# Kernel tuning notes

Measured on AMD Instinct MI355X. Metric: run time of the kernel, lower is better.

## Reference

```python
import jax, jax.numpy as jnp
import numpy as np

B, S, D = 8, 1024, 768
H, DH = 8, 96          # number_of_heads, head_outdim = D // H
DFF = 4 * D            # mlp hidden
EPS = 1e-5


def _p(key, shape, scale=0.02):
    return (jax.random.normal(key, shape, dtype=jnp.float32) * scale)


def setup_inputs() -> dict:
    key = jax.random.key(0)
    ks = jax.random.split(key, 16)
    return {
        "h": jax.random.normal(ks[0], (B, S, D), dtype=jnp.float32),
        "x": jax.random.normal(ks[1], (B, S, D), dtype=jnp.float32),
        # SLN 1: scalar gamma/beta + LayerNorm affine
        "g1": jnp.ones((), jnp.float32), "be1": jnp.zeros((), jnp.float32),
        "ln1_w": jnp.ones((D,), jnp.float32), "ln1_b": jnp.zeros((D,), jnp.float32),
        # SLN 2
        "g2": jnp.ones((), jnp.float32), "be2": jnp.zeros((), jnp.float32),
        "ln2_w": jnp.ones((D,), jnp.float32), "ln2_b": jnp.zeros((D,), jnp.float32),
        # MSA projections (stored as [in, out] for x @ W)
        "Wq": _p(ks[2], (D, H * DH)), "bq": jnp.zeros((H * DH,), jnp.float32),
        "Wk": _p(ks[3], (D, H * DH)), "bk": jnp.zeros((H * DH,), jnp.float32),
        "Wv": _p(ks[4], (D, H * DH)), "bv": jnp.zeros((H * DH,), jnp.float32),
        "Wo": _p(ks[5], (H * DH, D)), "bo": jnp.zeros((D,), jnp.float32),
        # MLP: D -> 4D -> D, relu
        "W1": _p(ks[6], (D, DFF)), "b1": jnp.zeros((DFF,), jnp.float32),
        "W2": _p(ks[7], (DFF, D)), "b2": jnp.zeros((D,), jnp.float32),
    }


def _sln(h, x, gamma, beta, w, b):
    # SLN(h, x) = gamma * x * LayerNorm(h) + beta * x
    mu = jnp.mean(h, axis=-1, keepdims=True)
    var = jnp.var(h, axis=-1, keepdims=True)
    ln = (h - mu) * jax.lax.rsqrt(var + EPS) * w + b
    return gamma * x * ln + beta * x


def _l2_msa(h, Wq, bq, Wk, bk, Wv, bv, Wo, bo):
    # L2-distance multi-head self-attention (lp=2)
    def heads(W, bias):
        y = h @ W + bias                      # [B,S,H*DH]
        return y.reshape(B, S, H, DH).transpose(0, 2, 1, 3)  # [B,H,S,DH]
    q, k, v = heads(Wq, bq), heads(Wk, bk), heads(Wv, bv)
    # pairwise L2 distances via the quadratic expansion (avoids [B,H,S,S,DH])
    q2 = jnp.sum(q * q, axis=-1)              # [B,H,S]
    k2 = jnp.sum(k * k, axis=-1)              # [B,H,S]
    qk = jnp.einsum("bhsd,bhtd->bhst", q, k)  # [B,H,S,S]
    d2 = jnp.maximum(q2[..., :, None] + k2[..., None, :] - 2.0 * qk, 0.0)
    dist = jnp.sqrt(d2)                       # cdist(q, k, p=2)
    attn = jax.nn.softmax(-dist / np.sqrt(DH), axis=-1)
    out = jnp.einsum("bhst,bhtd->bhsd", attn, v)  # [B,H,S,DH]
    out = out.transpose(0, 2, 1, 3).reshape(B, S, H * DH)
    return out @ Wo + bo


def reference(h, x, g1, be1, ln1_w, ln1_b, g2, be2, ln2_w, ln2_b,
              Wq, bq, Wk, bk, Wv, bv, Wo, bo, W1, b1, W2, b2):
    h1 = _sln(h, x, g1, be1, ln1_w, ln1_b)
    htmp = _l2_msa(h1, Wq, bq, Wk, bk, Wv, bv, Wo, bo) + h   # dropout_rate=0 -> identity
    h2 = _sln(htmp, x, g2, be2, ln2_w, ln2_b)
    hf = jax.nn.relu(h2 @ W1 + b1) @ W2 + b2 + htmp
    return (x, hf)
```

## Files before the change

### kernel.cpp

```cpp
#include <hip/hip_runtime.h>
#include <math.h>

#define B_ 8
#define S_ 1024
#define D_ 768
#define H_ 8
#define DH_ 96
#define DFF_ 3072
#define NTOK (B_*S_)
#define QKVW 2304
#define EPS_ 1e-5f

typedef __attribute__((ext_vector_type(4))) float f4;
typedef __attribute__((ext_vector_type(4))) int i4;
typedef __attribute__((ext_vector_type(8))) __bf16 bf16x8;
typedef __attribute__((ext_vector_type(4))) unsigned short us4;
typedef __attribute__((ext_vector_type(8))) unsigned short us8;

static __device__ __forceinline__ unsigned short f2bf(float f) {
    unsigned int u = __builtin_bit_cast(unsigned int, f);
    u += 0x7fffu + ((u >> 16) & 1u);
    return (unsigned short)(u >> 16);
}
static __device__ __forceinline__ float bf2f(unsigned short u) {
    unsigned int x = ((unsigned int)u) << 16;
    return __builtin_bit_cast(float, x);
}

#define GLOBAL_LOAD_LDS16(g, l) \
    __builtin_amdgcn_global_load_lds((const __attribute__((address_space(1))) unsigned int*)(g), \
                                     (__attribute__((address_space(3))) unsigned int*)(l), 16, 0, 0)

__global__ __launch_bounds__(192) void sln_kernel(
    const float* __restrict__ h, const float* __restrict__ x,
    const float* __restrict__ gamma, const float* __restrict__ beta,
    const float* __restrict__ w, const float* __restrict__ bvec,
    unsigned short* __restrict__ out_bf, float* __restrict__ xcopy)
{
    int row = blockIdx.x;
    int t = threadIdx.x;
    const float4* h4 = (const float4*)(h + (size_t)row * D_);
    const float4* x4 = (const float4*)(x + (size_t)row * D_);
    float4 hv = h4[t];
    float s  = hv.x + hv.y + hv.z + hv.w;
    float ss = hv.x*hv.x + hv.y*hv.y + hv.z*hv.z + hv.w*hv.w;
    #pragma unroll
    for (int off = 32; off > 0; off >>= 1) {
        s  += __shfl_down(s, off);
        ss += __shfl_down(ss, off);
    }
    __shared__ float red[2][3];
    int wid = t >> 6;
    if ((t & 63) == 0) { red[0][wid] = s; red[1][wid] = ss; }
    __syncthreads();
    float sum   = red[0][0] + red[0][1] + red[0][2];
    float sumsq = red[1][0] + red[1][1] + red[1][2];
    float mu  = sum * (1.0f / D_);
    float var = sumsq * (1.0f / D_) - mu * mu;
    float rstd = rsqrtf(var + EPS_);
    float g = gamma[0], be = beta[0];
    float4 wv = ((const float4*)w)[t];
    float4 bv = ((const float4*)bvec)[t];
    float4 xv = x4[t];
    us4 o;
    o.x = f2bf(xv.x * (g * ((hv.x - mu) * rstd * wv.x + bv.x) + be));
    o.y = f2bf(xv.y * (g * ((hv.y - mu) * rstd * wv.y + bv.y) + be));
    o.z = f2bf(xv.z * (g * ((hv.z - mu) * rstd * wv.z + bv.z) + be));
    o.w = f2bf(xv.w * (g * ((hv.w - mu) * rstd * wv.w + bv.w) + be));
    *(us4*)(out_bf + (size_t)row * D_ + t * 4) = o;
    if (xcopy) ((float4*)(xcopy + (size_t)row * D_))[t] = xv;
}

__global__ __launch_bounds__(256) void prep_all_kernel(
    const float* __restrict__ Wq, const float* __restrict__ Wk,
    const float* __restrict__ Wv, const float* __restrict__ Wo,
    const float* __restrict__ W1, const float* __restrict__ W2,
    const float* __restrict__ bq, const float* __restrict__ bk, const float* __restrict__ bv,
    unsigned short* __restrict__ Wqkvt, unsigned short* __restrict__ Wot,
    unsigned short* __restrict__ W1t, unsigned short* __restrict__ W2t,
    float* __restrict__ bqkv)
{
    int id = blockIdx.x;
    int tx = threadIdx.x, ty = threadIdx.y;
    if (id >= 6912) {
        int i = (id - 6912) * 256 + ty * 32 + tx;
        if (i < QKVW) {
            float v = (i < 768) ? bq[i] : (i < 1536) ? -2.f * bk[i - 768] : bv[i - 1536];
            bqkv[i] = v;
        }
        return;
    }
    const float* in; unsigned short* out; int K, N, nbx, rel;
    float scl = 1.f;
    if (id < 1728)      { int m = id / 576; rel = id % 576;
                          in = (m == 0) ? Wq : (m == 1) ? Wk : Wv;
                          if (m == 1) scl = -2.f;
                          out = Wqkvt + (size_t)m * 768 * 768; K = 768; N = 768; nbx = 24; }
    else if (id < 2304) { rel = id - 1728; in = Wo; out = Wot;  K = 768;  N = 768;  nbx = 24; }
    else if (id < 4608) { rel = id - 2304; in = W1; out = W1t;  K = 768;  N = 3072; nbx = 96; }
    else                { rel = id - 4608; in = W2; out = W2t;  K = 3072; N = 768;  nbx = 24; }
    int n0 = (rel % nbx) * 32, k0 = (rel / nbx) * 32;
    __shared__ float tile[32][33];
    #pragma unroll
    for (int r = 0; r < 4; r++)
        tile[ty + r * 8][tx] = in[(size_t)(k0 + ty + r * 8) * N + n0 + tx];
    __syncthreads();
    #pragma unroll
    for (int r = 0; r < 4; r++)
        out[(size_t)(n0 + ty + r * 8) * K + k0 + tx] = f2bf(scl * tile[tx][ty + r * 8]);
}

template<int OUT_BF16, int RELU>
__global__ __launch_bounds__(256) void gemm_mfma_kernel(
    const unsigned short* __restrict__ A, const unsigned short* __restrict__ Bt,
    const float* __restrict__ bias, const float* __restrict__ resid,
    void* __restrict__ Cout, int M, int N, int K)
{
    __shared__ unsigned short Asm[2][128 * 32];
    __shared__ unsigned short Bsm[2][128 * 32];

    int t = threadIdx.x;
    int lane = t & 63, wv = t >> 6;
    int wm = wv & 1, wn = wv >> 1;
    int l16 = lane & 15, quad = lane >> 4;

    int bm = blockIdx.x * 128;
    int bn = blockIdx.y * 128;

    const unsigned short* Abase = A  + (size_t)bm * K;
    const unsigned short* Bbase = Bt + (size_t)bn * K;

    int fl0 = t, fl1 = 256 + t;
    int r0 = fl0 >> 2, lg0 = (fl0 ^ (fl0 >> 3)) & 3;
    int r1 = fl1 >> 2, lg1 = (fl1 ^ (fl1 >> 3)) & 3;

    f4 acc[4][4] = {};

    GLOBAL_LOAD_LDS16(Abase + (size_t)r0 * K + lg0 * 8, &Asm[0][fl0 * 8]);
    GLOBAL_LOAD_LDS16(Abase + (size_t)r1 * K + lg1 * 8, &Asm[0][fl1 * 8]);
    GLOBAL_LOAD_LDS16(Bbase + (size_t)r0 * K + lg0 * 8, &Bsm[0][fl0 * 8]);
    GLOBAL_LOAD_LDS16(Bbase + (size_t)r1 * K + lg1 * 8, &Bsm[0][fl1 * 8]);
    __syncthreads();

    int nk = K >> 5;
    int cur = 0;
    for (int it = 0; it < nk; ++it) {
        if (it + 1 < nk) {
            int k0 = (it + 1) << 5;
            GLOBAL_LOAD_LDS16(Abase + (size_t)r0 * K + k0 + lg0 * 8, &Asm[cur ^ 1][fl0 * 8]);
            GLOBAL_LOAD_LDS16(Abase + (size_t)r1 * K + k0 + lg1 * 8, &Asm[cur ^ 1][fl1 * 8]);
            GLOBAL_LOAD_LDS16(Bbase + (size_t)r0 * K + k0 + lg0 * 8, &Bsm[cur ^ 1][fl0 * 8]);
            GLOBAL_LOAD_LDS16(Bbase + (size_t)r1 * K + k0 + lg1 * 8, &Bsm[cur ^ 1][fl1 * 8]);
        }

        bf16x8 xf[4], wf[4];
        #pragma unroll
        for (int i = 0; i < 4; i++) {
            int m = wm * 64 + i * 16 + l16;
            int p = (quad ^ (m >> 1)) & 3;
            xf[i] = __builtin_bit_cast(bf16x8, *(const i4*)&Asm[cur][m * 32 + p * 8]);
        }
        #pragma unroll
        for (int j = 0; j < 4; j++) {
            int n = wn * 64 + j * 16 + l16;
            int p = (quad ^ (n >> 1)) & 3;
            wf[j] = __builtin_bit_cast(bf16x8, *(const i4*)&Bsm[cur][n * 32 + p * 8]);
        }
        #pragma unroll
        for (int j = 0; j < 4; j++)
            #pragma unroll
            for (int i = 0; i < 4; i++)
                acc[j][i] = __builtin_amdgcn_mfma_f32_16x16x32_bf16(wf[j], xf[i], acc[j][i], 0, 0, 0);

        __syncthreads();
        cur ^= 1;
    }

    #pragma unroll
    for (int i = 0; i < 4; i++) {
        int rowg = bm + wm * 64 + i * 16 + l16;
        #pragma unroll
        for (int j = 0; j < 4; j++) {
            int colg0 = bn + wn * 64 + j * 16 + quad * 4;
            f4 v = acc[j][i];
            f4 b4 = *(const f4*)&bias[colg0];
            v += b4;
            if (RELU) {
                #pragma unroll
                for (int r = 0; r < 4; r++) v[r] = fmaxf(v[r], 0.f);
            }
            if (resid) {
                f4 r4 = *(const f4*)&resid[(size_t)rowg * N + colg0];
                v += r4;
            }
            if (OUT_BF16) {
                us4 o;
                o.x = f2bf(v[0]); o.y = f2bf(v[1]); o.z = f2bf(v[2]); o.w = f2bf(v[3]);
                *(us4*)((unsigned short*)Cout + (size_t)rowg * N + colg0) = o;
            } else {
                *(f4*)((float*)Cout + (size_t)rowg * N + colg0) = v;
            }
        }
    }
}

template<int OUT_BF16, int RELU>
__global__ __launch_bounds__(256) void gemm_mfma_n64_kernel(
    const unsigned short* __restrict__ A, const unsigned short* __restrict__ Bt,
    const float* __restrict__ bias, const float* __restrict__ resid,
    void* __restrict__ Cout, int M, int N, int K)
{
    __shared__ unsigned short Asm[2][128 * 64];
    __shared__ unsigned short Bsm[2][64 * 64];

    int t = threadIdx.x;
    int lane = t & 63, wv = t >> 6;
    int wm = wv & 1, wn = wv >> 1;
    int l16 = lane & 15, quad = lane >> 4;

    int bm = blockIdx.x * 128;
    int bn = blockIdx.y * 64;

    const unsigned short* Abase = A  + (size_t)bm * K;
    const unsigned short* Bbase = Bt + (size_t)bn * K;

    int ar[4], alg[4], br[2], blg[2];
    #pragma unroll
    for (int i = 0; i < 4; i++) {
        int fl = t + i * 256;
        ar[i] = fl >> 3; alg[i] = (fl ^ (fl >> 3)) & 7;
    }
    #pragma unroll
    for (int i = 0; i < 2; i++) {
        int fl = t + i * 256;
        br[i] = fl >> 3; blg[i] = (fl ^ (fl >> 3)) & 7;
    }

    f4 acc[2][4] = {};

    #pragma unroll
    for (int i = 0; i < 4; i++)
        GLOBAL_LOAD_LDS16(Abase + (size_t)ar[i] * K + alg[i] * 8, &Asm[0][(t + i * 256) * 8]);
    #pragma unroll
    for (int i = 0; i < 2; i++)
        GLOBAL_LOAD_LDS16(Bbase + (size_t)br[i] * K + blg[i] * 8, &Bsm[0][(t + i * 256) * 8]);
    __syncthreads();

    int nk = K >> 6;
    int cur = 0;
    for (int it = 0; it < nk; ++it) {
        if (it + 1 < nk) {
            int k0 = (it + 1) << 6;
            #pragma unroll
            for (int i = 0; i < 4; i++)
                GLOBAL_LOAD_LDS16(Abase + (size_t)ar[i] * K + k0 + alg[i] * 8, &Asm[cur ^ 1][(t + i * 256) * 8]);
            #pragma unroll
            for (int i = 0; i < 2; i++)
                GLOBAL_LOAD_LDS16(Bbase + (size_t)br[i] * K + k0 + blg[i] * 8, &Bsm[cur ^ 1][(t + i * 256) * 8]);
        }

        #pragma unroll
        for (int kk = 0; kk < 2; kk++) {
            bf16x8 xf[4], wf[2];
            #pragma unroll
            for (int i = 0; i < 4; i++) {
                int m = wm * 64 + i * 16 + l16;
                int p = ((kk * 4 + quad) ^ (m & 7)) & 7;
                xf[i] = __builtin_bit_cast(bf16x8, *(const i4*)&Asm[cur][m * 64 + p * 8]);
            }
            #pragma unroll
            for (int j = 0; j < 2; j++) {
                int n = wn * 32 + j * 16 + l16;
                int p = ((kk * 4 + quad) ^ (n & 7)) & 7;
                wf[j] = __builtin_bit_cast(bf16x8, *(const i4*)&Bsm[cur][n * 64 + p * 8]);
            }
            #pragma unroll
            for (int j = 0; j < 2; j++)
                #pragma unroll
                for (int i = 0; i < 4; i++)
                    acc[j][i] = __builtin_amdgcn_mfma_f32_16x16x32_bf16(wf[j], xf[i], acc[j][i], 0, 0, 0);
        }

        __syncthreads();
        cur ^= 1;
    }

    #pragma unroll
    for (int i = 0; i < 4; i++) {
        int rowg = bm + wm * 64 + i * 16 + l16;
        #pragma unroll
        for (int j = 0; j < 2; j++) {
            int colg0 = bn + wn * 32 + j * 16 + quad * 4;
            f4 v = acc[j][i];
            f4 b4 = *(const f4*)&bias[colg0];
            v += b4;
            if (RELU) {
                #pragma unroll
                for (int r = 0; r < 4; r++) v[r] = fmaxf(v[r], 0.f);
            }
            if (resid) {
                f4 r4 = *(const f4*)&resid[(size_t)rowg * N + colg0];
                v += r4;
            }
            if (OUT_BF16) {
                us4 o;
                o.x = f2bf(v[0]); o.y = f2bf(v[1]); o.z = f2bf(v[2]); o.w = f2bf(v[3]);
                *(us4*)((unsigned short*)Cout + (size_t)rowg * N + colg0) = o;
            } else {
                *(f4*)((float*)Cout + (size_t)rowg * N + colg0) = v;
            }
        }
    }
}

__global__ __launch_bounds__(256) void norms_kernel(
    const unsigned short* __restrict__ qkv, float* __restrict__ q2g, float* __restrict__ k2g)
{
    int row = blockIdx.x;
    int t = threadIdx.x;
    int hh = t >> 5, l32 = t & 31;
    const unsigned short* base = qkv + (size_t)row * QKVW + hh * DH_ + l32 * 3;
    float qs = 0.f, ks = 0.f;
    #pragma unroll
    for (int e = 0; e < 3; e++) {
        float qv = bf2f(base[e]);
        float kv = bf2f(base[768 + e]);
        qs += qv * qv; ks += kv * kv;
    }
    #pragma unroll
    for (int off = 16; off > 0; off >>= 1) {
        qs += __shfl_xor(qs, off, 32);
        ks += __shfl_xor(ks, off, 32);
    }
    if (l32 == 0) {
        int b = row >> 10, s = row & 1023;
        int idx = (b * H_ + hh) * S_ + s;
        q2g[idx] = qs; k2g[idx] = ks * 0.25f;
    }
}

__global__ __launch_bounds__(256) void vtrans_kernel(
    const unsigned short* __restrict__ qkv, unsigned short* __restrict__ vt)
{
    __shared__ unsigned short Vl[64][100];
    int blk = blockIdx.x;
    int bh = blk >> 4, kt = blk & 15;
    int b = bh >> 3, hh = bh & 7;
    int t = threadIdx.x;
    int key = t >> 2, qc = t & 3;
    const unsigned short* src = qkv + ((size_t)(b * S_ + kt * 64 + key)) * QKVW + 1536 + hh * DH_;
    #pragma unroll
    for (int i = 0; i < 3; i++) {
        int chunk = qc + i * 4;
        us8 v = *(const us8*)(src + chunk * 8);
        #pragma unroll
        for (int e = 0; e < 8; e++) Vl[key][chunk * 8 + e] = v[e];
    }
    __syncthreads();
    unsigned short* dst = vt + (size_t)blk * 7168;
    #pragma unroll
    for (int r = 0; r < 3; r++) {
        int c = r * 256 + t;
        int vd = c >> 3, kc = c & 7;
        us8 o;
        #pragma unroll
        for (int j = 0; j < 8; j++) o[j] = Vl[kc * 8 + j][vd];
        *(us8*)(dst + vd * 72 + kc * 8) = o;
    }
}

__global__ __launch_bounds__(256, 4) void attn_mfma_kernel(
    const unsigned short* __restrict__ qkv,
    const unsigned short* __restrict__ vt,
    const float* __restrict__ q2g, const float* __restrict__ k2g,
    unsigned short* __restrict__ outb)
{
    __shared__ unsigned short Klds[64 * 96];
    __shared__ unsigned short Vlds[7168];
    __shared__ unsigned short Plds[4][16 * 72];

    int t = threadIdx.x;
    int lane = t & 63, w = t >> 6;
    int l16 = lane & 15, quad = lane >> 4;

    int bid = blockIdx.x;
    int slot = bid >> 3;
    int bh = (bid & 7) * 8 + (slot >> 4);
    int qt = slot & 15;
    int b = bh >> 3, hh = bh & 7;

    int qrow0 = qt * 64 + w * 16;

    const unsigned short* qb = qkv + ((size_t)(b * S_ + qrow0)) * QKVW + hh * DH_;
    bf16x8 qf[3];
    #pragma unroll
    for (int d = 0; d < 3; d++)
        qf[d] = __builtin_bit_cast(bf16x8,
            *(const i4*)(qb + (size_t)l16 * QKVW + d * 32 + quad * 8));

    float q2n = q2g[bh * S_ + qrow0 + l16];

    float lsum = 0.f;
    f4 Oacc[6] = {};

    const float cexp = 0.14724445f;

    const unsigned short* kgb = qkv + ((size_t)(b * S_)) * QKVW + 768 + hh * DH_;
    const unsigned short* vgb0 = vt + (size_t)(bh * 16) * 7168;
    const float* k2base = k2g + bh * S_;

    for (int it = 0; it < 16; it++) {
        float4 k2f[4];
        #pragma unroll
        for (int kt2 = 0; kt2 < 4; kt2++)
            k2f[kt2] = *(const float4*)(k2base + it * 64 + kt2 * 16 + quad * 4);

        __syncthreads();
        #pragma unroll
        for (int r = 0; r < 3; r++) {
            int c = r * 256 + t;
            int key = c & 63, dc = c >> 6;
            GLOBAL_LOAD_LDS16(kgb + ((size_t)(it * 64 + key)) * QKVW + dc * 8, &Klds[c * 8]);
        }
        const unsigned short* vgb = vgb0 + (size_t)it * 7168;
        #pragma unroll
        for (int r = 0; r < 3; r++)
            GLOBAL_LOAD_LDS16(vgb + (r * 256 + t) * 8, &Vlds[(r * 256 + t) * 8]);
        if (t < 128)
            GLOBAL_LOAD_LDS16(vgb + (768 + t) * 8, &Vlds[(768 + t) * 8]);
        __syncthreads();

        const unsigned short* kB = &Klds[quad * 512 + l16 * 8];
        #pragma unroll
        for (int kt2 = 0; kt2 < 4; kt2++) {
            const unsigned short* kp = kB + kt2 * 128;
            bf16x8 kf0 = __builtin_bit_cast(bf16x8, *(const i4*)(kp));
            bf16x8 kf1 = __builtin_bit_cast(bf16x8, *(const i4*)(kp + 2048));
            bf16x8 kf2 = __builtin_bit_cast(bf16x8, *(const i4*)(kp + 4096));
            f4 a = {k2f[kt2].x + q2n, k2f[kt2].y + q2n, k2f[kt2].z + q2n, k2f[kt2].w + q2n};
            a = __builtin_amdgcn_mfma_f32_16x16x32_bf16(kf0, qf[0], a, 0, 0, 0);
            a = __builtin_amdgcn_mfma_f32_16x16x32_bf16(kf1, qf[1], a, 0, 0, 0);
            a = __builtin_amdgcn_mfma_f32_16x16x32_bf16(kf2, qf[2], a, 0, 0, 0);
            #pragma unroll
            for (int r2 = 0; r2 < 4; r2++) {
                float d2 = fmaxf(a[r2], 0.f);
                float p = exp2f(-__builtin_amdgcn_sqrtf(d2) * cexp);
                lsum += p;
                a[r2] = p;
            }
            unsigned int plo, phi;
            asm("v_cvt_pk_bf16_f32 %0, %1, %2" : "=v"(plo) : "v"(a[0]), "v"(a[1]));
            asm("v_cvt_pk_bf16_f32 %0, %1, %2" : "=v"(phi) : "v"(a[2]), "v"(a[3]));
            uint2 pkd; pkd.x = plo; pkd.y = phi;
            *(uint2*)&Plds[w][l16 * 72 + kt2 * 16 + quad * 4] = pkd;
        }
        bf16x8 pa0 = __builtin_bit_cast(bf16x8, *(const i4*)&Plds[w][l16 * 72 + quad * 8]);
        bf16x8 pa1 = __builtin_bit_cast(bf16x8, *(const i4*)&Plds[w][l16 * 72 + 32 + quad * 8]);
        #pragma unroll
        for (int vtl = 0; vtl < 6; vtl++) {
            bf16x8 vf0 = __builtin_bit_cast(bf16x8, *(const i4*)&Vlds[(vtl * 16 + l16) * 72 + quad * 8]);
            bf16x8 vf1 = __builtin_bit_cast(bf16x8, *(const i4*)&Vlds[(vtl * 16 + l16) * 72 + 32 + quad * 8]);
            Oacc[vtl] = __builtin_amdgcn_mfma_f32_16x16x32_bf16(pa0, vf0, Oacc[vtl], 0, 0, 0);
            Oacc[vtl] = __builtin_amdgcn_mfma_f32_16x16x32_bf16(pa1, vf1, Oacc[vtl], 0, 0, 0);
        }
    }
    lsum += __shfl_xor(lsum, 16, 64);
    lsum += __shfl_xor(lsum, 32, 64);
    float inv_l = 1.f / lsum;
    f4 iv;
    #pragma unroll
    for (int r2 = 0; r2 < 4; r2++)
        iv[r2] = __shfl(inv_l, quad * 4 + r2, 64);
    #pragma unroll
    for (int vtl = 0; vtl < 6; vtl++)
        #pragma unroll
        for (int r2 = 0; r2 < 4; r2++) {
            int row = b * S_ + qrow0 + quad * 4 + r2;
            outb[(size_t)row * D_ + hh * DH_ + vtl * 16 + l16] = f2bf(Oacc[vtl][r2] * iv[r2]);
        }
}

extern "C" void kernel_launch(void* const* d_in, const int* in_sizes, int n_in,
                              void* d_out, int out_size, void* d_ws, size_t ws_size,
                              hipStream_t stream)
{
    const float* h    = (const float*)d_in[0];
    const float* x    = (const float*)d_in[1];
    const float* g1   = (const float*)d_in[2];
    const float* be1  = (const float*)d_in[3];
    const float* ln1w = (const float*)d_in[4];
    const float* ln1b = (const float*)d_in[5];
    const float* g2   = (const float*)d_in[6];
    const float* be2  = (const float*)d_in[7];
    const float* ln2w = (const float*)d_in[8];
    const float* ln2b = (const float*)d_in[9];
    const float* Wq   = (const float*)d_in[10];
    const float* bq   = (const float*)d_in[11];
    const float* Wk   = (const float*)d_in[12];
    const float* bk   = (const float*)d_in[13];
    const float* Wv   = (const float*)d_in[14];
    const float* bv   = (const float*)d_in[15];
    const float* Wo   = (const float*)d_in[16];
    const float* bo   = (const float*)d_in[17];
    const float* W1   = (const float*)d_in[18];
    const float* b1   = (const float*)d_in[19];
    const float* W2   = (const float*)d_in[20];
    const float* b2   = (const float*)d_in[21];

    float* out = (float*)d_out;
    char* wsb = (char*)d_ws;
    const size_t ND = (size_t)NTOK * D_;

    size_t off = 0;
    unsigned short* W1t = (unsigned short*)(wsb + off); off += 4718592;
    unsigned short* W2t = (unsigned short*)(wsb + off); off += 4718592;
    float* bqkv = (float*)(wsb + off);                  off += 16384;
    float* htmp = (float*)(wsb + off);                  off += ND * 4;
    float* q2g  = (float*)(wsb + off);                  off += (size_t)B_ * H_ * S_ * 4;
    float* k2g  = (float*)(wsb + off);                  off += (size_t)B_ * H_ * S_ * 4;
    unsigned short* h2b = (unsigned short*)(wsb + off); off += ND * 2;
    size_t pool0 = off;
    unsigned short* Wqkvt = (unsigned short*)(wsb + off); off += 3538944;
    unsigned short* Wot   = (unsigned short*)(wsb + off); off += 1179648;
    unsigned short* h1b   = (unsigned short*)(wsb + off); off += ND * 2;
    unsigned short* vtg   = (unsigned short*)(wsb + off); off += (size_t)1024 * 14336;
    unsigned short* qkvb  = (unsigned short*)(wsb + off); off += (size_t)NTOK * QKVW * 2;
    unsigned short* attnb   = h1b;
    unsigned short* hiddenb = (unsigned short*)(wsb + pool0);

    prep_all_kernel<<<6921, dim3(32, 8), 0, stream>>>(
        Wq, Wk, Wv, Wo, W1, W2, bq, bk, bv, Wqkvt, Wot, W1t, W2t, bqkv);

    sln_kernel<<<NTOK, 192, 0, stream>>>(h, x, g1, be1, ln1w, ln1b, h1b, out);

    gemm_mfma_kernel<1, 0><<<dim3(NTOK/128, QKVW/128), 256, 0, stream>>>(
        h1b, Wqkvt, bqkv, nullptr, qkvb, NTOK, QKVW, D_);

    norms_kernel<<<NTOK, 256, 0, stream>>>(qkvb, q2g, k2g);
    vtrans_kernel<<<1024, 256, 0, stream>>>(qkvb, vtg);

    attn_mfma_kernel<<<1024, 256, 0, stream>>>(qkvb, vtg, q2g, k2g, attnb);

    gemm_mfma_n64_kernel<0, 0><<<dim3(NTOK/128, D_/64), 256, 0, stream>>>(
        attnb, Wot, bo, h, htmp, NTOK, D_, D_);

    sln_kernel<<<NTOK, 192, 0, stream>>>(htmp, x, g2, be2, ln2w, ln2b, h2b, nullptr);

    gemm_mfma_kernel<1, 1><<<dim3(NTOK/128, DFF_/128), 256, 0, stream>>>(
        h2b, W1t, b1, nullptr, hiddenb, NTOK, DFF_, D_);
    gemm_mfma_n64_kernel<0, 0><<<dim3(NTOK/128, D_/64), 256, 0, stream>>>(
        hiddenb, W2t, b2, htmp, out + ND, NTOK, D_, DFF_);

    (void)in_sizes; (void)n_in; (void)out_size; (void)ws_size;
}
```

Before: 429.3 us.

## Double-buffer K/V tiles and process two query fragments per wave in attention

The L2 attention kernel now has each wave handle 32 query rows (two 16-row fragments), so each K/V tile loaded into LDS is reused across twice as many queries and the grid is halved to 512 blocks. K and V tiles are double-buffered, with the next tile's global-to-LDS load issued before computing on the current one, which removes one barrier per iteration and overlaps loads with compute. The cost is more registers (launch bounds relaxed to 2 blocks per SM), more LDS per block, and fewer blocks in flight.

```diff
diff --git a/kernel.cpp b/kernel.cpp
--- a/kernel.cpp
+++ b/kernel.cpp
@@ -369,15 +369,15 @@
     }
 }
 
-__global__ __launch_bounds__(256, 4) void attn_mfma_kernel(
+__global__ __launch_bounds__(256, 2) void attn_mfma_kernel(
     const unsigned short* __restrict__ qkv,
     const unsigned short* __restrict__ vt,
     const float* __restrict__ q2g, const float* __restrict__ k2g,
     unsigned short* __restrict__ outb)
 {
-    __shared__ unsigned short Klds[64 * 96];
-    __shared__ unsigned short Vlds[7168];
-    __shared__ unsigned short Plds[4][16 * 72];
+    __shared__ unsigned short Klds[2][6144];
+    __shared__ unsigned short Vlds[2][7168];
+    __shared__ unsigned short Plds[4][2][16 * 72];
 
     int t = threadIdx.x;
     int lane = t & 63, w = t >> 6;
@@ -385,23 +385,28 @@
 
     int bid = blockIdx.x;
     int slot = bid >> 3;
-    int bh = (bid & 7) * 8 + (slot >> 4);
-    int qt = slot & 15;
+    int bh = (bid & 7) * 8 + (slot >> 3);
+    int qt = slot & 7;
     int b = bh >> 3, hh = bh & 7;
 
-    int qrow0 = qt * 64 + w * 16;
-
-    const unsigned short* qb = qkv + ((size_t)(b * S_ + qrow0)) * QKVW + hh * DH_;
-    bf16x8 qf[3];
-    #pragma unroll
-    for (int d = 0; d < 3; d++)
-        qf[d] = __builtin_bit_cast(bf16x8,
-            *(const i4*)(qb + (size_t)l16 * QKVW + d * 32 + quad * 8));
-
-    float q2n = q2g[bh * S_ + qrow0 + l16];
-
-    float lsum = 0.f;
-    f4 Oacc[6] = {};
+    int qrowW = qt * 128 + w * 32;
+
+    const unsigned short* qb = qkv + ((size_t)(b * S_ + qrowW)) * QKVW + hh * DH_;
+    bf16x8 qf[2][3];
+    #pragma unroll
+    for (int f = 0; f < 2; f++)
+        #pragma unroll
+        for (int d = 0; d < 3; d++)
+            qf[f][d] = __builtin_bit_cast(bf16x8,
+                *(const i4*)(qb + (size_t)(f * 16 + l16) * QKVW + d * 32 + quad * 8));
+
+    float q2n[2];
+    #pragma unroll
+    for (int f = 0; f < 2; f++)
+        q2n[f] = q2g[bh * S_ + qrowW + f * 16 + l16];
+
+    float lsum0 = 0.f, lsum1 = 0.f;
+    f4 Oacc[2][6] = {};
 
     const float cexp = 0.14724445f;
 
@@ -409,75 +414,101 @@
     const unsigned short* vgb0 = vt + (size_t)(bh * 16) * 7168;
     const float* k2base = k2g + bh * S_;
 
+    int kkey = t & 63;
+    #define ATTN_STAGE(bb, itv)                                                   \
+        {                                                                         \
+            _Pragma("unroll")                                                     \
+            for (int r = 0; r < 3; r++) {                                         \
+                int c = r * 256 + t;                                              \
+                int dc = c >> 6;                                                  \
+                GLOBAL_LOAD_LDS16(kgb + ((size_t)((itv) * 64 + kkey)) * QKVW + dc * 8, \
+                                  &Klds[bb][c * 8]);                              \
+            }                                                                     \
+            const unsigned short* vgb = vgb0 + (size_t)(itv) * 7168;              \
+            _Pragma("unroll")                                                     \
+            for (int r = 0; r < 3; r++)                                           \
+                GLOBAL_LOAD_LDS16(vgb + (r * 256 + t) * 8, &Vlds[bb][(r * 256 + t) * 8]); \
+            if (t < 128)                                                          \
+                GLOBAL_LOAD_LDS16(vgb + (768 + t) * 8, &Vlds[bb][(768 + t) * 8]); \
+        }
+
+    ATTN_STAGE(0, 0);
+    __syncthreads();
+
     for (int it = 0; it < 16; it++) {
+        int cur = it & 1;
+        if (it) __syncthreads();
+        if (it + 1 < 16) ATTN_STAGE(cur ^ 1, it + 1);
+
         float4 k2f[4];
         #pragma unroll
         for (int kt2 = 0; kt2 < 4; kt2++)
             k2f[kt2] = *(const float4*)(k2base + it * 64 + kt2 * 16 + quad * 4);
 
-        __syncthreads();
-        #pragma unroll
-        for (int r = 0; r < 3; r++) {
-            int c = r * 256 + t;
-            int key = c & 63, dc = c >> 6;
-            GLOBAL_LOAD_LDS16(kgb + ((size_t)(it * 64 + key)) * QKVW + dc * 8, &Klds[c * 8]);
-        }
-        const unsigned short* vgb = vgb0 + (size_t)it * 7168;
-        #pragma unroll
-        for (int r = 0; r < 3; r++)
-            GLOBAL_LOAD_LDS16(vgb + (r * 256 + t) * 8, &Vlds[(r * 256 + t) * 8]);
-        if (t < 128)
-            GLOBAL_LOAD_LDS16(vgb + (768 + t) * 8, &Vlds[(768 + t) * 8]);
-        __syncthreads();
-
-        const unsigned short* kB = &Klds[quad * 512 + l16 * 8];
+        const unsigned short* kB = &Klds[cur][quad * 512 + l16 * 8];
         #pragma unroll
         for (int kt2 = 0; kt2 < 4; kt2++) {
             const unsigned short* kp = kB + kt2 * 128;
             bf16x8 kf0 = __builtin_bit_cast(bf16x8, *(const i4*)(kp));
             bf16x8 kf1 = __builtin_bit_cast(bf16x8, *(const i4*)(kp + 2048));
             bf16x8 kf2 = __builtin_bit_cast(bf16x8, *(const i4*)(kp + 4096));
-            f4 a = {k2f[kt2].x + q2n, k2f[kt2].y + q2n, k2f[kt2].z + q2n, k2f[kt2].w + q2n};
-            a = __builtin_amdgcn_mfma_f32_16x16x32_bf16(kf0, qf[0], a, 0, 0, 0);
-            a = __builtin_amdgcn_mfma_f32_16x16x32_bf16(kf1, qf[1], a, 0, 0, 0);
-            a = __builtin_amdgcn_mfma_f32_16x16x32_bf16(kf2, qf[2], a, 0, 0, 0);
+            #pragma unroll
+            for (int f = 0; f < 2; f++) {
+                f4 a = {k2f[kt2].x + q2n[f], k2f[kt2].y + q2n[f],
+                        k2f[kt2].z + q2n[f], k2f[kt2].w + q2n[f]};
+                a = __builtin_amdgcn_mfma_f32_16x16x32_bf16(kf0, qf[f][0], a, 0, 0, 0);
+                a = __builtin_amdgcn_mfma_f32_16x16x32_bf16(kf1, qf[f][1], a, 0, 0, 0);
+                a = __builtin_amdgcn_mfma_f32_16x16x32_bf16(kf2, qf[f][2], a, 0, 0, 0);
+                #pragma unroll
+                for (int r2 = 0; r2 < 4; r2++) {
+                    float d2 = fmaxf(a[r2], 0.f);
+                    float p = exp2f(-__builtin_amdgcn_sqrtf(d2) * cexp);
+                    if (f == 0) lsum0 += p; else lsum1 += p;
+                    a[r2] = p;
+                }
+                unsigned int plo, phi;
+                asm("v_cvt_pk_bf16_f32 %0, %1, %2" : "=v"(plo) : "v"(a[0]), "v"(a[1]));
+                asm("v_cvt_pk_bf16_f32 %0, %1, %2" : "=v"(phi) : "v"(a[2]), "v"(a[3]));
+                uint2 pkd; pkd.x = plo; pkd.y = phi;
+                *(uint2*)&Plds[w][f][l16 * 72 + kt2 * 16 + quad * 4] = pkd;
+            }
+        }
+        bf16x8 pa[2][2];
+        #pragma unroll
+        for (int f = 0; f < 2; f++) {
+            pa[f][0] = __builtin_bit_cast(bf16x8, *(const i4*)&Plds[w][f][l16 * 72 + quad * 8]);
+            pa[f][1] = __builtin_bit_cast(bf16x8, *(const i4*)&Plds[w][f][l16 * 72 + 32 + quad * 8]);
+        }
+        #pragma unroll
+        for (int vtl = 0; vtl < 6; vtl++) {
+            bf16x8 vf0 = __builtin_bit_cast(bf16x8, *(const i4*)&Vlds[cur][(vtl * 16 + l16) * 72 + quad * 8]);
+            bf16x8 vf1 = __builtin_bit_cast(bf16x8, *(const i4*)&Vlds[cur][(vtl * 16 + l16) * 72 + 32 + quad * 8]);
+            #pragma unroll
+            for (int f = 0; f < 2; f++) {
+                Oacc[f][vtl] = __builtin_amdgcn_mfma_f32_16x16x32_bf16(pa[f][0], vf0, Oacc[f][vtl], 0, 0, 0);
+                Oacc[f][vtl] = __builtin_amdgcn_mfma_f32_16x16x32_bf16(pa[f][1], vf1, Oacc[f][vtl], 0, 0, 0);
+            }
+        }
+    }
+    #pragma unroll
+    for (int f = 0; f < 2; f++) {
+        float ls = (f == 0) ? lsum0 : lsum1;
+        ls += __shfl_xor(ls, 16, 64);
+        ls += __shfl_xor(ls, 32, 64);
+        float inv_l = 1.f / ls;
+        f4 iv;
+        #pragma unroll
+        for (int r2 = 0; r2 < 4; r2++)
+            iv[r2] = __shfl(inv_l, quad * 4 + r2, 64);
+        #pragma unroll
+        for (int vtl = 0; vtl < 6; vtl++)
             #pragma unroll
             for (int r2 = 0; r2 < 4; r2++) {
-                float d2 = fmaxf(a[r2], 0.f);
-                float p = exp2f(-__builtin_amdgcn_sqrtf(d2) * cexp);
-                lsum += p;
-                a[r2] = p;
-            }
-            unsigned int plo, phi;
-            asm("v_cvt_pk_bf16_f32 %0, %1, %2" : "=v"(plo) : "v"(a[0]), "v"(a[1]));
-            asm("v_cvt_pk_bf16_f32 %0, %1, %2" : "=v"(phi) : "v"(a[2]), "v"(a[3]));
-            uint2 pkd; pkd.x = plo; pkd.y = phi;
-            *(uint2*)&Plds[w][l16 * 72 + kt2 * 16 + quad * 4] = pkd;
-        }
-        bf16x8 pa0 = __builtin_bit_cast(bf16x8, *(const i4*)&Plds[w][l16 * 72 + quad * 8]);
-        bf16x8 pa1 = __builtin_bit_cast(bf16x8, *(const i4*)&Plds[w][l16 * 72 + 32 + quad * 8]);
-        #pragma unroll
-        for (int vtl = 0; vtl < 6; vtl++) {
-            bf16x8 vf0 = __builtin_bit_cast(bf16x8, *(const i4*)&Vlds[(vtl * 16 + l16) * 72 + quad * 8]);
-            bf16x8 vf1 = __builtin_bit_cast(bf16x8, *(const i4*)&Vlds[(vtl * 16 + l16) * 72 + 32 + quad * 8]);
-            Oacc[vtl] = __builtin_amdgcn_mfma_f32_16x16x32_bf16(pa0, vf0, Oacc[vtl], 0, 0, 0);
-            Oacc[vtl] = __builtin_amdgcn_mfma_f32_16x16x32_bf16(pa1, vf1, Oacc[vtl], 0, 0, 0);
-        }
-    }
-    lsum += __shfl_xor(lsum, 16, 64);
-    lsum += __shfl_xor(lsum, 32, 64);
-    float inv_l = 1.f / lsum;
-    f4 iv;
-    #pragma unroll
-    for (int r2 = 0; r2 < 4; r2++)
-        iv[r2] = __shfl(inv_l, quad * 4 + r2, 64);
-    #pragma unroll
-    for (int vtl = 0; vtl < 6; vtl++)
-        #pragma unroll
-        for (int r2 = 0; r2 < 4; r2++) {
-            int row = b * S_ + qrow0 + quad * 4 + r2;
-            outb[(size_t)row * D_ + hh * DH_ + vtl * 16 + l16] = f2bf(Oacc[vtl][r2] * iv[r2]);
-        }
+                int row = b * S_ + qrowW + f * 16 + quad * 4 + r2;
+                outb[(size_t)row * D_ + hh * DH_ + vtl * 16 + l16] = f2bf(Oacc[f][vtl][r2] * iv[r2]);
+            }
+    }
+    #undef ATTN_STAGE
 }
 
 extern "C" void kernel_launch(void* const* d_in, const int* in_sizes, int n_in,
@@ -539,7 +570,7 @@
     norms_kernel<<<NTOK, 256, 0, stream>>>(qkvb, q2g, k2g);
     vtrans_kernel<<<1024, 256, 0, stream>>>(qkvb, vtg);
 
-    attn_mfma_kernel<<<1024, 256, 0, stream>>>(qkvb, vtg, q2g, k2g, attnb);
+    attn_mfma_kernel<<<512, 256, 0, stream>>>(qkvb, vtg, q2g, k2g, attnb);
 
     gemm_mfma_n64_kernel<0, 0><<<dim3(NTOK/128, D_/64), 256, 0, stream>>>(
         attnb, Wot, bo, h, htmp, NTOK, D_, D_);
```

Result: no change. 425.1 us (-1.0%).
